# Kernel optimization log

Measured on AMD Instinct MI355X. Metric: run time of the kernel, lower is better.

The kernel has to match this reference:

```python
import jax, jax.numpy as jnp
import numpy as np


def setup_inputs() -> dict:
    key = jax.random.key(0)
    k1, k2, k3, k4 = jax.random.split(key, 4)
    N, E, C_in, C_out = 100000, 1600000, 256, 128
    x = jax.random.normal(k1, (N, C_in), dtype=jnp.float32)
    edge_index = jax.random.randint(k2, (2, E), 0, N, dtype=jnp.int64)
    W = jax.random.normal(k3, (C_in, C_out), dtype=jnp.float32) * 0.05
    b = jax.random.normal(k4, (C_out,), dtype=jnp.float32) * 0.05
    return {"x": x, "edge_index": edge_index, "W": W, "b": b}


def reference(x, edge_index, W, b):
    # GCNConv (PyG defaults): add self-loops, symmetric normalization,
    # linear transform, scatter-sum aggregation, bias; then ReLU (norm=None).
    N = x.shape[0]
    loops = jnp.arange(N, dtype=edge_index.dtype)
    src = jnp.concatenate([edge_index[0], loops])  # [E+N] message sources (x_j)
    dst = jnp.concatenate([edge_index[1], loops])  # [E+N] aggregation targets

    deg = jax.ops.segment_sum(jnp.ones_like(dst, dtype=x.dtype), dst, num_segments=N)
    deg_inv_sqrt = jnp.where(deg > 0, jax.lax.rsqrt(jnp.maximum(deg, 1.0)), 0.0)
    norm = deg_inv_sqrt[src] * deg_inv_sqrt[dst]  # [E+N]

    h = x @ W                                      # [N, C_out]
    msg = h[src] * norm[:, None]                   # [E+N, C_out] gather + scale
    out = jax.ops.segment_sum(msg, dst, num_segments=N) + b  # scatter-add
    return jax.nn.relu(out)
```

## Files before the change

### kernel.cpp

```cpp
#include <hip/hip_runtime.h>


typedef __attribute__((ext_vector_type(8))) short bf16x8;
typedef __attribute__((ext_vector_type(4))) float f32x4;
typedef __attribute__((ext_vector_type(2))) unsigned int u32x2;

__device__ __forceinline__ unsigned short f2bf(float f) {
  unsigned int u = __float_as_uint(f);
  u += 0x7FFFu + ((u >> 16) & 1u);
  return (unsigned short)(u >> 16);
}
__device__ __forceinline__ float bfval(unsigned short h) {
  return __uint_as_float(((unsigned int)h) << 16);
}
__device__ __forceinline__ float bf0(unsigned int u) { return __uint_as_float(u << 16); }
__device__ __forceinline__ float bf1(unsigned int u) { return __uint_as_float(u & 0xFFFF0000u); }

#define EPB 4096
#define MAXB 256

__global__ __launch_bounds__(256) void k_prep_bin(
    const float* __restrict__ W, unsigned short* __restrict__ blob,
    const int* __restrict__ src, const int* __restrict__ dst,
    u32x2* __restrict__ pairs, unsigned int* __restrict__ binTail,
    int E, int nbins, int shift, int cap)
{
  __shared__ u32x2 stg[EPB];
  __shared__ unsigned int lcnt[MAXB], lbase[MAXB], loff[MAXB];

  const int tid = threadIdx.x;
  const int id = blockIdx.x;

  if (id < 128) {
    int g = id * 256 + tid;
    int k = g >> 7, c = g & 127;
    float w = W[g];
    unsigned short hi = f2bf(w);
    unsigned short lo = f2bf(w - bfval(hi));
    int q = k >> 5, kk = k & 31;
    unsigned lin = (unsigned)(c * 64 + kk * 2);
    unsigned swz = lin ^ (((unsigned)(c & 7)) << 4);
    blob[(q * 16384 + swz) >> 1] = hi;
    blob[(q * 16384 + 8192 + swz) >> 1] = lo;
    return;
  }

  const int e0 = (id - 128) * EPB;
  for (int i = tid; i < MAXB; i += 256) { lcnt[i] = 0u; loff[i] = 0u; }
  __syncthreads();

  #pragma unroll
  for (int i = 0; i < EPB / 256; ++i) {
    const int e = e0 + i * 256 + tid;
    u32x2 pr = {0xFFFFFFFFu, 0u};
    if (e < E) {
      int d = __builtin_nontemporal_load(dst + e);
      int s = __builtin_nontemporal_load(src + e);
      pr.x = (unsigned)d; pr.y = (unsigned)s;
      atomicAdd(&lcnt[d >> shift], 1u);
    }
    stg[i * 256 + tid] = pr;
  }
  __syncthreads();

  if (tid < nbins) {
    unsigned c = lcnt[tid];
    lbase[tid] = c ? atomicAdd(&binTail[tid], c) : 0u;
  }
  __syncthreads();

  #pragma unroll
  for (int i = 0; i < EPB / 256; ++i) {
    const u32x2 pr = stg[i * 256 + tid];
    if (pr.x != 0xFFFFFFFFu) {
      const int bin = (int)(pr.x >> shift);
      const unsigned p = lbase[bin] + atomicAdd(&loff[bin], 1u);
      if (p < (unsigned)cap) {
        u32x2 o;
        o.x = pr.x - ((unsigned)bin << shift);
        o.y = pr.y;
        __builtin_nontemporal_store(o, pairs + (size_t)bin * cap + p);
      }
    }
  }
}

__global__ __launch_bounds__(256) void k_gemm_scatter(
    const float* __restrict__ x, const unsigned char* __restrict__ wblob,
    unsigned short* __restrict__ h, int N,
    const u32x2* __restrict__ pairs, const unsigned int* __restrict__ binTail,
    unsigned int* __restrict__ cnt, int* __restrict__ srcs,
    int nbins, int shift, int cap, int gemmB)
{
  __shared__ __align__(16) unsigned char smem[20480];

  const int id = blockIdx.x;
  const int tid = threadIdx.x;

  if (id < nbins) {
    unsigned int* lcnt = (unsigned int*)smem;
    const int bin = id;
    const int bsz = 1 << shift;
    const int nbase = bin << shift;
    const int nn = min(bsz, N - nbase);
    if (nn <= 0) return;
    for (int i = tid; i < bsz; i += 256) lcnt[i] = 0u;
    __syncthreads();
    const int n = min((int)binTail[bin], cap);
    const u32x2* bp = pairs + (size_t)bin * cap;
    for (int p = tid; p < n; p += 256) {
      const u32x2 pr = bp[p];
      const unsigned pos = atomicAdd(&lcnt[pr.x], 1u);
      if (pos < 64)
        srcs[(((size_t)(nbase + pr.x)) << 6) + pos] = (int)pr.y;
    }
    __syncthreads();
    for (int i = tid; i < nn; i += 256) cnt[nbase + i] = lcnt[i];
    return;
  }

  const int idx = id - nbins;
  if (idx >= gemmB) return;

  const int row0 = idx * 32;
  const int lane = tid & 63;
  const int wv = tid >> 6;
  const int mb = wv & 1;
  const int nb = wv >> 1;

  f32x4 acc[4] = {};

  const int ar = tid >> 3;
  const int akk0 = (tid & 7) * 4;
  int arow = row0 + ar; if (arow >= N) arow = N - 1;
  const unsigned aaddr = ((unsigned)(ar * 64 + akk0 * 2)) ^ (((unsigned)(ar & 7)) << 4);

  const int rr = 16 * mb + (lane & 15);
  const unsigned aoff = ((unsigned)(rr * 64 + (lane >> 4) * 16)) ^ (((unsigned)(rr & 7)) << 4);

  for (int q = 0; q < 8; ++q) {
    {
      const f32x4 v = __builtin_nontemporal_load(
          (const f32x4*)(x + (size_t)arow * 256 + q * 32 + akk0));
      unsigned short h0 = f2bf(v[0]), h1 = f2bf(v[1]), h2 = f2bf(v[2]), h3 = f2bf(v[3]);
      unsigned short l0 = f2bf(v[0] - bfval(h0));
      unsigned short l1 = f2bf(v[1] - bfval(h1));
      unsigned short l2 = f2bf(v[2] - bfval(h2));
      unsigned short l3 = f2bf(v[3] - bfval(h3));
      *(uint2*)(smem + 16384 + aaddr) =
          make_uint2((unsigned)h0 | ((unsigned)h1 << 16), (unsigned)h2 | ((unsigned)h3 << 16));
      *(uint2*)(smem + 18432 + aaddr) =
          make_uint2((unsigned)l0 | ((unsigned)l1 << 16), (unsigned)l2 | ((unsigned)l3 << 16));
    }
    {
      const uint4* gb = (const uint4*)(wblob + (size_t)q * 16384);
      uint4* sb = (uint4*)smem;
      uint4 t0 = gb[tid], t1 = gb[tid + 256], t2 = gb[tid + 512], t3 = gb[tid + 768];
      sb[tid] = t0; sb[tid + 256] = t1; sb[tid + 512] = t2; sb[tid + 768] = t3;
    }
    __syncthreads();
    {
      const bf16x8 ah = *(const bf16x8*)(smem + 16384 + aoff);
      const bf16x8 al = *(const bf16x8*)(smem + 18432 + aoff);
      #pragma unroll
      for (int nf = 0; nf < 4; ++nf) {
        const int c = 64 * nb + 16 * nf + (lane & 15);
        const unsigned boff =
            ((unsigned)(c * 64 + (lane >> 4) * 16)) ^ (((unsigned)(c & 7)) << 4);
        const bf16x8 bh = *(const bf16x8*)(smem + boff);
        const bf16x8 bl = *(const bf16x8*)(smem + 8192 + boff);
        acc[nf] = __builtin_amdgcn_mfma_f32_16x16x32_bf16(ah, bh, acc[nf], 0, 0, 0);
        acc[nf] = __builtin_amdgcn_mfma_f32_16x16x32_bf16(ah, bl, acc[nf], 0, 0, 0);
        acc[nf] = __builtin_amdgcn_mfma_f32_16x16x32_bf16(al, bh, acc[nf], 0, 0, 0);
      }
    }
    __syncthreads();
  }

  #pragma unroll
  for (int nf = 0; nf < 4; ++nf) {
    const int col = 64 * nb + 16 * nf + (lane & 15);
    #pragma unroll
    for (int r = 0; r < 4; ++r) {
      const int row = row0 + 16 * mb + 4 * (lane >> 4) + r;
      if (row < N) h[(size_t)row * 128 + col] = f2bf(acc[nf][r]);
    }
  }
}

__global__ __launch_bounds__(256) void k_aggr(
    const unsigned short* __restrict__ h, const int* __restrict__ srcs,
    const unsigned int* __restrict__ cnt,
    const float* __restrict__ b, float* __restrict__ out, int N)
{
  const int wid = (int)(((size_t)blockIdx.x * 256 + threadIdx.x) >> 6);
  if (wid >= N) return;
  const int lane = threadIdx.x & 63;
  const int eg = lane >> 4;
  const int cl = lane & 15;
  const int deg = min((int)cnt[wid], 64);
  const int m = deg + 1;
  const size_t coff = (size_t)(cl << 3);
  const size_t lbase = (size_t)wid << 6;

  float a0 = 0.f, a1 = 0.f, a2 = 0.f, a3 = 0.f, a4 = 0.f, a5 = 0.f, a6 = 0.f, a7 = 0.f;

  for (int base = 0; base < m; base += 64) {
    const int kk = min(64, m - base);
    const int slot = base + lane;
    int sidx = wid;
    if (slot < deg) sidx = srcs[lbase + slot];
    const float sd = rsqrtf((float)(cnt[sidx] + 1u));
    int j = 0;
    for (; j + 8 <= kk; j += 8) {
      const int s0 = __shfl(sidx, j + eg, 64);
      const int s1 = __shfl(sidx, j + 4 + eg, 64);
      const float d0 = __shfl(sd, j + eg, 64);
      const float d1 = __shfl(sd, j + 4 + eg, 64);
      const uint4 v0 = *(const uint4*)(h + ((size_t)s0 << 7) + coff);
      const uint4 v1 = *(const uint4*)(h + ((size_t)s1 << 7) + coff);
      a0 = fmaf(bf0(v0.x), d0, a0); a1 = fmaf(bf1(v0.x), d0, a1);
      a2 = fmaf(bf0(v0.y), d0, a2); a3 = fmaf(bf1(v0.y), d0, a3);
      a4 = fmaf(bf0(v0.z), d0, a4); a5 = fmaf(bf1(v0.z), d0, a5);
      a6 = fmaf(bf0(v0.w), d0, a6); a7 = fmaf(bf1(v0.w), d0, a7);
      a0 = fmaf(bf0(v1.x), d1, a0); a1 = fmaf(bf1(v1.x), d1, a1);
      a2 = fmaf(bf0(v1.y), d1, a2); a3 = fmaf(bf1(v1.y), d1, a3);
      a4 = fmaf(bf0(v1.z), d1, a4); a5 = fmaf(bf1(v1.z), d1, a5);
      a6 = fmaf(bf0(v1.w), d1, a6); a7 = fmaf(bf1(v1.w), d1, a7);
    }
    for (; j < kk; j += 4) {
      const int s0 = __shfl(sidx, j + eg, 64);
      const float d0 = __shfl(sd, j + eg, 64);
      if (j + eg < kk) {
        const uint4 v0 = *(const uint4*)(h + ((size_t)s0 << 7) + coff);
        a0 = fmaf(bf0(v0.x), d0, a0); a1 = fmaf(bf1(v0.x), d0, a1);
        a2 = fmaf(bf0(v0.y), d0, a2); a3 = fmaf(bf1(v0.y), d0, a3);
        a4 = fmaf(bf0(v0.z), d0, a4); a5 = fmaf(bf1(v0.z), d0, a5);
        a6 = fmaf(bf0(v0.w), d0, a6); a7 = fmaf(bf1(v0.w), d0, a7);
      }
    }
  }

  a0 += __shfl_xor(a0, 16, 64); a0 += __shfl_xor(a0, 32, 64);
  a1 += __shfl_xor(a1, 16, 64); a1 += __shfl_xor(a1, 32, 64);
  a2 += __shfl_xor(a2, 16, 64); a2 += __shfl_xor(a2, 32, 64);
  a3 += __shfl_xor(a3, 16, 64); a3 += __shfl_xor(a3, 32, 64);
  a4 += __shfl_xor(a4, 16, 64); a4 += __shfl_xor(a4, 32, 64);
  a5 += __shfl_xor(a5, 16, 64); a5 += __shfl_xor(a5, 32, 64);
  a6 += __shfl_xor(a6, 16, 64); a6 += __shfl_xor(a6, 32, 64);
  a7 += __shfl_xor(a7, 16, 64); a7 += __shfl_xor(a7, 32, 64);

  if (lane < 32) {
    const float dn = rsqrtf((float)m);
    const int hi = lane >> 4;
    const int c0 = ((lane & 15) << 3) + (hi << 2);
    const float4 bb = *(const float4*)(b + c0);
    const float r0 = hi ? a4 : a0;
    const float r1 = hi ? a5 : a1;
    const float r2 = hi ? a6 : a2;
    const float r3 = hi ? a7 : a3;
    float4 o;
    o.x = fmaxf(fmaf(dn, r0, bb.x), 0.f);
    o.y = fmaxf(fmaf(dn, r1, bb.y), 0.f);
    o.z = fmaxf(fmaf(dn, r2, bb.z), 0.f);
    o.w = fmaxf(fmaf(dn, r3, bb.w), 0.f);
    *(float4*)(out + ((size_t)wid << 7) + c0) = o;
  }
}

extern "C" void kernel_launch(void* const* d_in, const int* in_sizes, int n_in,
                              void* d_out, int out_size, void* d_ws, size_t ws_size,
                              hipStream_t stream)
{
  const float* x  = (const float*)d_in[0];
  const int* ei   = (const int*)d_in[1];
  const float* W  = (const float*)d_in[2];
  const float* b  = (const float*)d_in[3];
  float* out = (float*)d_out;

  const int Cout = in_sizes[3];
  const int Cin  = in_sizes[2] / Cout;
  const int N    = in_sizes[0] / Cin;
  const int E    = in_sizes[1] / 2;

  const int* src = ei;
  const int* dst = ei + E;

  int shift = 9;
  while (((N + (1 << shift) - 1) >> shift) > MAXB) ++shift;
  const int nbins = (N + (1 << shift) - 1) >> shift;
  const int cap = E / nbins + E / (2 * nbins) + 1024;

  char* p = (char*)d_ws;
  size_t off = 0;
  auto alloc = [&](size_t bytes) { char* q = p + off; off = (off + bytes + 255) & ~(size_t)255; return q; };
  unsigned int* cnt = (unsigned int*)alloc((size_t)N * 4);
  int* srcs         = (int*)alloc((size_t)N * 64 * 4);
  unsigned short* h = (unsigned short*)alloc((size_t)N * Cout * 2);
  unsigned short* wblob = (unsigned short*)alloc(8 * 16384);
  unsigned int* binTail = (unsigned int*)alloc((size_t)nbins * 4);
  u32x2* pairs      = (u32x2*)alloc((size_t)nbins * cap * 8);

  const int gemmB = (N + 31) / 32;
  const int binB  = (E + EPB - 1) / EPB;

  (void)hipMemsetAsync(binTail, 0, (size_t)nbins * 4, stream);
  k_prep_bin<<<128 + binB, 256, 0, stream>>>(W, wblob, src, dst,
                                             pairs, binTail, E, nbins, shift, cap);
  k_gemm_scatter<<<nbins + gemmB, 256, 0, stream>>>(x, (const unsigned char*)wblob, h, N,
                                                    pairs, binTail, cnt, srcs,
                                                    nbins, shift, cap, gemmB);
  k_aggr<<<(N + 3) / 4, 256, 0, stream>>>(h, srcs, cnt, b, out, N);
}
```

Measured before the change: 337.2 us.

## Fuse memset, prep/bin and gemm/scatter into one cooperative persistent kernel

Merges the binTail memset, the weight-prep/edge-binning kernel and the gemm/bucket kernel into a single cooperative kernel of 1024 persistent blocks, separated by grid-wide syncs. It also splits the per-block bin histogram into per-wavefront copies to reduce LDS atomic contention, and re-reads dst/src from global memory instead of staging edge pairs in LDS. The goal is to remove launch gaps and the memset. In exchange it adds grid barriers and a fixed grid size that may underfill or serialize work, and it keeps the old kernels as a fallback if the cooperative launch fails.

Measured after the change: 691.1 us. 2.05x slower.

```diff
diff --git a/kernel.cpp b/kernel.cpp
--- a/kernel.cpp
+++ b/kernel.cpp
@@ -1,4 +1,7 @@
 #include <hip/hip_runtime.h>
+#include <hip/hip_cooperative_groups.h>
+
+namespace cg = cooperative_groups;
 
 
 typedef __attribute__((ext_vector_type(8))) short bf16x8;
@@ -19,109 +22,50 @@
 #define EPB 4096
 #define MAXB 256
 
-__global__ __launch_bounds__(256) void k_prep_bin(
-    const float* __restrict__ W, unsigned short* __restrict__ blob,
-    const int* __restrict__ src, const int* __restrict__ dst,
-    u32x2* __restrict__ pairs, unsigned int* __restrict__ binTail,
-    int E, int nbins, int shift, int cap)
-{
-  __shared__ u32x2 stg[EPB];
-  __shared__ unsigned int lcnt[MAXB], lbase[MAXB], loff[MAXB];
-
-  const int tid = threadIdx.x;
-  const int id = blockIdx.x;
-
-  if (id < 128) {
-    int g = id * 256 + tid;
-    int k = g >> 7, c = g & 127;
-    float w = W[g];
-    unsigned short hi = f2bf(w);
-    unsigned short lo = f2bf(w - bfval(hi));
-    int q = k >> 5, kk = k & 31;
-    unsigned lin = (unsigned)(c * 64 + kk * 2);
-    unsigned swz = lin ^ (((unsigned)(c & 7)) << 4);
-    blob[(q * 16384 + swz) >> 1] = hi;
-    blob[(q * 16384 + 8192 + swz) >> 1] = lo;
-    return;
-  }
-
-  const int e0 = (id - 128) * EPB;
-  for (int i = tid; i < MAXB; i += 256) { lcnt[i] = 0u; loff[i] = 0u; }
-  __syncthreads();
-
-  #pragma unroll
-  for (int i = 0; i < EPB / 256; ++i) {
-    const int e = e0 + i * 256 + tid;
-    u32x2 pr = {0xFFFFFFFFu, 0u};
-    if (e < E) {
-      int d = __builtin_nontemporal_load(dst + e);
-      int s = __builtin_nontemporal_load(src + e);
-      pr.x = (unsigned)d; pr.y = (unsigned)s;
-      atomicAdd(&lcnt[d >> shift], 1u);
-    }
-    stg[i * 256 + tid] = pr;
-  }
-  __syncthreads();
-
-  if (tid < nbins) {
-    unsigned c = lcnt[tid];
-    lbase[tid] = c ? atomicAdd(&binTail[tid], c) : 0u;
-  }
-  __syncthreads();
-
-  #pragma unroll
-  for (int i = 0; i < EPB / 256; ++i) {
-    const u32x2 pr = stg[i * 256 + tid];
-    if (pr.x != 0xFFFFFFFFu) {
-      const int bin = (int)(pr.x >> shift);
-      const unsigned p = lbase[bin] + atomicAdd(&loff[bin], 1u);
-      if (p < (unsigned)cap) {
-        u32x2 o;
-        o.x = pr.x - ((unsigned)bin << shift);
-        o.y = pr.y;
-        __builtin_nontemporal_store(o, pairs + (size_t)bin * cap + p);
-      }
-    }
-  }
-}
-
-__global__ __launch_bounds__(256) void k_gemm_scatter(
-    const float* __restrict__ x, const unsigned char* __restrict__ wblob,
-    unsigned short* __restrict__ h, int N,
+
+__device__ __forceinline__ void wprep_elem(const float* __restrict__ W,
+                                           unsigned short* __restrict__ blob, int g) {
+  int k = g >> 7, c = g & 127;
+  float w = W[g];
+  unsigned short hi = f2bf(w);
+  unsigned short lo = f2bf(w - bfval(hi));
+  int q = k >> 5, kk = k & 31;
+  unsigned lin = (unsigned)(c * 64 + kk * 2);
+  unsigned swz = lin ^ (((unsigned)(c & 7)) << 4);
+  blob[(q * 16384 + swz) >> 1] = hi;
+  blob[(q * 16384 + 8192 + swz) >> 1] = lo;
+}
+
+__device__ __forceinline__ void bucket_body(
+    unsigned char* smem, int bin, int tid,
     const u32x2* __restrict__ pairs, const unsigned int* __restrict__ binTail,
     unsigned int* __restrict__ cnt, int* __restrict__ srcs,
-    int nbins, int shift, int cap, int gemmB)
-{
-  __shared__ __align__(16) unsigned char smem[20480];
-
-  const int id = blockIdx.x;
-  const int tid = threadIdx.x;
-
-  if (id < nbins) {
-    unsigned int* lcnt = (unsigned int*)smem;
-    const int bin = id;
-    const int bsz = 1 << shift;
-    const int nbase = bin << shift;
-    const int nn = min(bsz, N - nbase);
-    if (nn <= 0) return;
-    for (int i = tid; i < bsz; i += 256) lcnt[i] = 0u;
-    __syncthreads();
-    const int n = min((int)binTail[bin], cap);
-    const u32x2* bp = pairs + (size_t)bin * cap;
-    for (int p = tid; p < n; p += 256) {
-      const u32x2 pr = bp[p];
-      const unsigned pos = atomicAdd(&lcnt[pr.x], 1u);
-      if (pos < 64)
-        srcs[(((size_t)(nbase + pr.x)) << 6) + pos] = (int)pr.y;
-    }
-    __syncthreads();
-    for (int i = tid; i < nn; i += 256) cnt[nbase + i] = lcnt[i];
-    return;
-  }
-
-  const int idx = id - nbins;
-  if (idx >= gemmB) return;
-
+    int N, int shift, int cap)
+{
+  unsigned int* lcnt = (unsigned int*)smem;
+  const int bsz = 1 << shift;
+  const int nbase = bin << shift;
+  const int nn = min(bsz, N - nbase);
+  if (nn <= 0) return;
+  for (int i = tid; i < bsz; i += 256) lcnt[i] = 0u;
+  __syncthreads();
+  const int n = min((int)binTail[bin], cap);
+  const u32x2* bp = pairs + (size_t)bin * cap;
+  for (int p = tid; p < n; p += 256) {
+    const u32x2 pr = bp[p];
+    const unsigned pos = atomicAdd(&lcnt[pr.x], 1u);
+    if (pos < 64)
+      srcs[(((size_t)(nbase + pr.x)) << 6) + pos] = (int)pr.y;
+  }
+  __syncthreads();
+  for (int i = tid; i < nn; i += 256) cnt[nbase + i] = lcnt[i];
+}
+
+__device__ __forceinline__ void gemm_body(
+    unsigned char* smem, int idx, int tid,
+    const float* __restrict__ x, const unsigned char* __restrict__ wblob,
+    unsigned short* __restrict__ h, int N)
+{
   const int row0 = idx * 32;
   const int lane = tid & 63;
   const int wv = tid >> 6;
@@ -186,6 +130,151 @@
       if (row < N) h[(size_t)row * 128 + col] = f2bf(acc[nf][r]);
     }
   }
+}
+
+__global__ __launch_bounds__(256) void k_mega(
+    const float* __restrict__ x, const float* __restrict__ W,
+    const int* __restrict__ src, const int* __restrict__ dst,
+    unsigned short* __restrict__ wblob, u32x2* __restrict__ pairs,
+    unsigned int* __restrict__ binTail, unsigned int* __restrict__ cnt,
+    int* __restrict__ srcs, unsigned short* __restrict__ h,
+    int N, int E, int nbins, int shift, int cap, int prepB, int gemmB)
+{
+  __shared__ __align__(16) unsigned char smem[20480];
+  cg::grid_group grid = cg::this_grid();
+  const int tid = threadIdx.x;
+  const int nblk = (int)gridDim.x;
+  const int gtid = (int)blockIdx.x * 256 + tid;
+  const int gthreads = nblk * 256;
+
+  for (int i = gtid; i < nbins; i += gthreads) binTail[i] = 0u;
+  for (int g = gtid; g < 256 * 128; g += gthreads) wprep_elem(W, wblob, g);
+  __threadfence();
+  grid.sync();
+
+  for (int vb = (int)blockIdx.x; vb < prepB; vb += nblk) {
+    unsigned int* lcnt4 = (unsigned int*)smem;
+    unsigned int* lbase = lcnt4 + 4 * MAXB;
+    unsigned int* loff  = lbase + MAXB;
+    __syncthreads();
+    for (int i = tid; i < 4 * MAXB; i += 256) lcnt4[i] = 0u;
+    for (int i = tid; i < MAXB; i += 256) loff[i] = 0u;
+    __syncthreads();
+    const int e0 = vb * EPB;
+    const int wv = tid >> 6;
+    #pragma unroll
+    for (int i = 0; i < EPB / 256; ++i) {
+      const int e = e0 + i * 256 + tid;
+      if (e < E) {
+        int d = __builtin_nontemporal_load(dst + e);
+        atomicAdd(&lcnt4[wv * MAXB + (d >> shift)], 1u);
+      }
+    }
+    __syncthreads();
+    if (tid < nbins) {
+      unsigned c = lcnt4[tid] + lcnt4[MAXB + tid] + lcnt4[2 * MAXB + tid] + lcnt4[3 * MAXB + tid];
+      lbase[tid] = c ? atomicAdd(&binTail[tid], c) : 0u;
+    }
+    __syncthreads();
+    #pragma unroll
+    for (int i = 0; i < EPB / 256; ++i) {
+      const int e = e0 + i * 256 + tid;
+      if (e < E) {
+        int d = dst[e];
+        int s = src[e];
+        const int bin = d >> shift;
+        const unsigned p = lbase[bin] + atomicAdd(&loff[bin], 1u);
+        if (p < (unsigned)cap) {
+          u32x2 o;
+          o.x = (unsigned)d - ((unsigned)bin << shift);
+          o.y = (unsigned)s;
+          __builtin_nontemporal_store(o, pairs + (size_t)bin * cap + p);
+        }
+      }
+    }
+  }
+  __threadfence();
+  grid.sync();
+
+  for (int vb = (int)blockIdx.x; vb < nbins + gemmB; vb += nblk) {
+    __syncthreads();
+    if (vb < nbins)
+      bucket_body(smem, vb, tid, pairs, binTail, cnt, srcs, N, shift, cap);
+    else
+      gemm_body(smem, vb - nbins, tid, x, (const unsigned char*)wblob, h, N);
+  }
+}
+
+
+__global__ __launch_bounds__(256) void k_prep_bin(
+    const float* __restrict__ W, unsigned short* __restrict__ blob,
+    const int* __restrict__ src, const int* __restrict__ dst,
+    u32x2* __restrict__ pairs, unsigned int* __restrict__ binTail,
+    int E, int nbins, int shift, int cap)
+{
+  __shared__ unsigned int lcnt4[4 * MAXB];
+  __shared__ unsigned int lbase[MAXB], loff[MAXB];
+  const int tid = threadIdx.x;
+  const int id = blockIdx.x;
+
+  if (id < 128) {
+    wprep_elem(W, blob, id * 256 + tid);
+    return;
+  }
+  for (int i = tid; i < 4 * MAXB; i += 256) lcnt4[i] = 0u;
+  for (int i = tid; i < MAXB; i += 256) loff[i] = 0u;
+  __syncthreads();
+  const int e0 = (id - 128) * EPB;
+  const int wv = tid >> 6;
+  #pragma unroll
+  for (int i = 0; i < EPB / 256; ++i) {
+    const int e = e0 + i * 256 + tid;
+    if (e < E) {
+      int d = __builtin_nontemporal_load(dst + e);
+      atomicAdd(&lcnt4[wv * MAXB + (d >> shift)], 1u);
+    }
+  }
+  __syncthreads();
+  if (tid < nbins) {
+    unsigned c = lcnt4[tid] + lcnt4[MAXB + tid] + lcnt4[2 * MAXB + tid] + lcnt4[3 * MAXB + tid];
+    lbase[tid] = c ? atomicAdd(&binTail[tid], c) : 0u;
+  }
+  __syncthreads();
+  #pragma unroll
+  for (int i = 0; i < EPB / 256; ++i) {
+    const int e = e0 + i * 256 + tid;
+    if (e < E) {
+      int d = dst[e];
+      int s = src[e];
+      const int bin = d >> shift;
+      const unsigned p = lbase[bin] + atomicAdd(&loff[bin], 1u);
+      if (p < (unsigned)cap) {
+        u32x2 o;
+        o.x = (unsigned)d - ((unsigned)bin << shift);
+        o.y = (unsigned)s;
+        __builtin_nontemporal_store(o, pairs + (size_t)bin * cap + p);
+      }
+    }
+  }
+}
+
+__global__ __launch_bounds__(256) void k_gemm_scatter(
+    const float* __restrict__ x, const unsigned char* __restrict__ wblob,
+    unsigned short* __restrict__ h, int N,
+    const u32x2* __restrict__ pairs, const unsigned int* __restrict__ binTail,
+    unsigned int* __restrict__ cnt, int* __restrict__ srcs,
+    int nbins, int shift, int cap, int gemmB)
+{
+  __shared__ __align__(16) unsigned char smem[20480];
+  const int id = blockIdx.x;
+  const int tid = threadIdx.x;
+  if (id < nbins) {
+    bucket_body(smem, id, tid, pairs, binTail, cnt, srcs, N, shift, cap);
+    return;
+  }
+  const int idx = id - nbins;
+  if (idx >= gemmB) return;
+  gemm_body(smem, idx, tid, x, wblob, h, N);
 }
 
 __global__ __launch_bounds__(256) void k_aggr(
@@ -302,13 +391,34 @@
   u32x2* pairs      = (u32x2*)alloc((size_t)nbins * cap * 8);
 
   const int gemmB = (N + 31) / 32;
-  const int binB  = (E + EPB - 1) / EPB;
-
-  (void)hipMemsetAsync(binTail, 0, (size_t)nbins * 4, stream);
-  k_prep_bin<<<128 + binB, 256, 0, stream>>>(W, wblob, src, dst,
-                                             pairs, binTail, E, nbins, shift, cap);
-  k_gemm_scatter<<<nbins + gemmB, 256, 0, stream>>>(x, (const unsigned char*)wblob, h, N,
-                                                    pairs, binTail, cnt, srcs,
-                                                    nbins, shift, cap, gemmB);
+  const int prepB = (E + EPB - 1) / EPB;
+
+  {
+    int N_ = N, E_ = E, nbins_ = nbins, shift_ = shift, cap_ = cap;
+    int prepB_ = prepB, gemmB_ = gemmB;
+    const float* x_ = x; const float* W_ = W;
+    const int* src_ = src; const int* dst_ = dst;
+    unsigned short* wblob_ = wblob; u32x2* pairs_ = pairs;
+    unsigned int* binTail_ = binTail; unsigned int* cnt_ = cnt;
+    int* srcs_ = srcs; unsigned short* h_ = h;
+    void* args[] = {
+      (void*)&x_, (void*)&W_, (void*)&src_, (void*)&dst_,
+      (void*)&wblob_, (void*)&pairs_, (void*)&binTail_, (void*)&cnt_,
+      (void*)&srcs_, (void*)&h_,
+      (void*)&N_, (void*)&E_, (void*)&nbins_, (void*)&shift_, (void*)&cap_,
+      (void*)&prepB_, (void*)&gemmB_
+    };
+    hipError_t err = hipLaunchCooperativeKernel((const void*)k_mega,
+                                                dim3(1024), dim3(256),
+                                                args, 0, stream);
+    if (err != hipSuccess) {
+      (void)hipMemsetAsync(binTail, 0, (size_t)nbins * 4, stream);
+      k_prep_bin<<<128 + prepB, 256, 0, stream>>>(W, wblob, src, dst,
+                                                  pairs, binTail, E, nbins, shift, cap);
+      k_gemm_scatter<<<nbins + gemmB, 256, 0, stream>>>(x, (const unsigned char*)wblob, h, N,
+                                                        pairs, binTail, cnt, srcs,
+                                                        nbins, shift, cap, gemmB);
+    }
+  }
   k_aggr<<<(N + 3) / 4, 256, 0, stream>>>(h, srcs, cnt, b, out, N);
 }
```

## Overlap edge binning with GEMM and split bucket pass into separate kernel

Applied to the files above, without the earlier changes.

Moves the edge-binning pass out of the W-prep kernel and co-schedules it with the GEMM blocks in one launch, so the memory-bound binning overlaps the MFMA work. The per-bin bucketing becomes its own kernel with 1024-thread blocks. Binning now keeps per-wave shared counters to reduce atomic contention, re-reads dst/src instead of staging them in LDS, and halves the edges per block. The output store becomes nontemporal. In exchange it adds a kernel launch and reads the edge indices twice.

New measurement: 343.9 us. No clear change (+2.0%).

```diff
diff --git a/kernel.cpp b/kernel.cpp
--- a/kernel.cpp
+++ b/kernel.cpp
@@ -16,110 +16,79 @@
 __device__ __forceinline__ float bf0(unsigned int u) { return __uint_as_float(u << 16); }
 __device__ __forceinline__ float bf1(unsigned int u) { return __uint_as_float(u & 0xFFFF0000u); }
 
-#define EPB 4096
+#define EPB 2048
 #define MAXB 256
 
-__global__ __launch_bounds__(256) void k_prep_bin(
-    const float* __restrict__ W, unsigned short* __restrict__ blob,
+__global__ __launch_bounds__(256) void k_wprep(
+    const float* __restrict__ W, unsigned short* __restrict__ blob)
+{
+  int g = blockIdx.x * 256 + threadIdx.x;
+  int k = g >> 7, c = g & 127;
+  float w = W[g];
+  unsigned short hi = f2bf(w);
+  unsigned short lo = f2bf(w - bfval(hi));
+  int q = k >> 5, kk = k & 31;
+  unsigned lin = (unsigned)(c * 64 + kk * 2);
+  unsigned swz = lin ^ (((unsigned)(c & 7)) << 4);
+  blob[(q * 16384 + swz) >> 1] = hi;
+  blob[(q * 16384 + 8192 + swz) >> 1] = lo;
+}
+
+__global__ __launch_bounds__(256) void k_work(
+    const float* __restrict__ x, const unsigned char* __restrict__ wblob,
+    unsigned short* __restrict__ h, int N,
     const int* __restrict__ src, const int* __restrict__ dst,
     u32x2* __restrict__ pairs, unsigned int* __restrict__ binTail,
-    int E, int nbins, int shift, int cap)
-{
-  __shared__ u32x2 stg[EPB];
-  __shared__ unsigned int lcnt[MAXB], lbase[MAXB], loff[MAXB];
-
-  const int tid = threadIdx.x;
-  const int id = blockIdx.x;
-
-  if (id < 128) {
-    int g = id * 256 + tid;
-    int k = g >> 7, c = g & 127;
-    float w = W[g];
-    unsigned short hi = f2bf(w);
-    unsigned short lo = f2bf(w - bfval(hi));
-    int q = k >> 5, kk = k & 31;
-    unsigned lin = (unsigned)(c * 64 + kk * 2);
-    unsigned swz = lin ^ (((unsigned)(c & 7)) << 4);
-    blob[(q * 16384 + swz) >> 1] = hi;
-    blob[(q * 16384 + 8192 + swz) >> 1] = lo;
-    return;
-  }
-
-  const int e0 = (id - 128) * EPB;
-  for (int i = tid; i < MAXB; i += 256) { lcnt[i] = 0u; loff[i] = 0u; }
-  __syncthreads();
-
-  #pragma unroll
-  for (int i = 0; i < EPB / 256; ++i) {
-    const int e = e0 + i * 256 + tid;
-    u32x2 pr = {0xFFFFFFFFu, 0u};
-    if (e < E) {
-      int d = __builtin_nontemporal_load(dst + e);
-      int s = __builtin_nontemporal_load(src + e);
-      pr.x = (unsigned)d; pr.y = (unsigned)s;
-      atomicAdd(&lcnt[d >> shift], 1u);
-    }
-    stg[i * 256 + tid] = pr;
-  }
-  __syncthreads();
-
-  if (tid < nbins) {
-    unsigned c = lcnt[tid];
-    lbase[tid] = c ? atomicAdd(&binTail[tid], c) : 0u;
-  }
-  __syncthreads();
-
-  #pragma unroll
-  for (int i = 0; i < EPB / 256; ++i) {
-    const u32x2 pr = stg[i * 256 + tid];
-    if (pr.x != 0xFFFFFFFFu) {
-      const int bin = (int)(pr.x >> shift);
-      const unsigned p = lbase[bin] + atomicAdd(&loff[bin], 1u);
-      if (p < (unsigned)cap) {
-        u32x2 o;
-        o.x = pr.x - ((unsigned)bin << shift);
-        o.y = pr.y;
-        __builtin_nontemporal_store(o, pairs + (size_t)bin * cap + p);
-      }
-    }
-  }
-}
-
-__global__ __launch_bounds__(256) void k_gemm_scatter(
-    const float* __restrict__ x, const unsigned char* __restrict__ wblob,
-    unsigned short* __restrict__ h, int N,
-    const u32x2* __restrict__ pairs, const unsigned int* __restrict__ binTail,
-    unsigned int* __restrict__ cnt, int* __restrict__ srcs,
-    int nbins, int shift, int cap, int gemmB)
+    int E, int nbins, int shift, int cap, int binB, int gemmB)
 {
   __shared__ __align__(16) unsigned char smem[20480];
 
   const int id = blockIdx.x;
   const int tid = threadIdx.x;
 
-  if (id < nbins) {
-    unsigned int* lcnt = (unsigned int*)smem;
-    const int bin = id;
-    const int bsz = 1 << shift;
-    const int nbase = bin << shift;
-    const int nn = min(bsz, N - nbase);
-    if (nn <= 0) return;
-    for (int i = tid; i < bsz; i += 256) lcnt[i] = 0u;
-    __syncthreads();
-    const int n = min((int)binTail[bin], cap);
-    const u32x2* bp = pairs + (size_t)bin * cap;
-    for (int p = tid; p < n; p += 256) {
-      const u32x2 pr = bp[p];
-      const unsigned pos = atomicAdd(&lcnt[pr.x], 1u);
-      if (pos < 64)
-        srcs[(((size_t)(nbase + pr.x)) << 6) + pos] = (int)pr.y;
-    }
-    __syncthreads();
-    for (int i = tid; i < nn; i += 256) cnt[nbase + i] = lcnt[i];
+  if (id < binB) {
+    unsigned int* lcnt4 = (unsigned int*)smem;
+    unsigned int* lbase = lcnt4 + 4 * MAXB;
+    unsigned int* loff  = lbase + MAXB;
+    for (int i = tid; i < 4 * MAXB; i += 256) lcnt4[i] = 0u;
+    for (int i = tid; i < MAXB; i += 256) loff[i] = 0u;
+    __syncthreads();
+    const int e0 = id * EPB;
+    const int wv = tid >> 6;
+    #pragma unroll
+    for (int i = 0; i < EPB / 256; ++i) {
+      const int e = e0 + i * 256 + tid;
+      if (e < E) {
+        int d = dst[e];
+        atomicAdd(&lcnt4[wv * MAXB + (d >> shift)], 1u);
+      }
+    }
+    __syncthreads();
+    if (tid < nbins) {
+      unsigned c = lcnt4[tid] + lcnt4[MAXB + tid] + lcnt4[2 * MAXB + tid] + lcnt4[3 * MAXB + tid];
+      lbase[tid] = c ? atomicAdd(&binTail[tid], c) : 0u;
+    }
+    __syncthreads();
+    #pragma unroll
+    for (int i = 0; i < EPB / 256; ++i) {
+      const int e = e0 + i * 256 + tid;
+      if (e < E) {
+        int d = dst[e];
+        int s = src[e];
+        const int bin = d >> shift;
+        const unsigned p = lbase[bin] + atomicAdd(&loff[bin], 1u);
+        if (p < (unsigned)cap) {
+          u32x2 o;
+          o.x = (unsigned)d - ((unsigned)bin << shift);
+          o.y = (unsigned)s;
+          __builtin_nontemporal_store(o, pairs + (size_t)bin * cap + p);
+        }
+      }
+    }
     return;
   }
 
-  const int idx = id - nbins;
+  const int idx = id - binB;
   if (idx >= gemmB) return;
 
   const int row0 = idx * 32;
@@ -186,6 +155,32 @@
       if (row < N) h[(size_t)row * 128 + col] = f2bf(acc[nf][r]);
     }
   }
+}
+
+__global__ __launch_bounds__(1024) void k_bucket(
+    const u32x2* __restrict__ pairs, const unsigned int* __restrict__ binTail,
+    unsigned int* __restrict__ cnt, int* __restrict__ srcs,
+    int N, int shift, int cap)
+{
+  __shared__ unsigned int lcnt[1 << 9];
+  const int bin = blockIdx.x;
+  const int tid = threadIdx.x;
+  const int bsz = 1 << shift;
+  const int nbase = bin << shift;
+  const int nn = min(bsz, N - nbase);
+  if (nn <= 0) return;
+  for (int i = tid; i < bsz; i += 1024) lcnt[i] = 0u;
+  __syncthreads();
+  const int n = min((int)binTail[bin], cap);
+  const u32x2* bp = pairs + (size_t)bin * cap;
+  for (int p = tid; p < n; p += 1024) {
+    const u32x2 pr = __builtin_nontemporal_load(bp + p);
+    const unsigned pos = atomicAdd(&lcnt[pr.x], 1u);
+    if (pos < 64)
+      srcs[(((size_t)(nbase + pr.x)) << 6) + pos] = (int)pr.y;
+  }
+  __syncthreads();
+  for (int i = tid; i < nn; i += 1024) cnt[nbase + i] = lcnt[i];
 }
 
 __global__ __launch_bounds__(256) void k_aggr(
@@ -259,12 +254,12 @@
     const float r1 = hi ? a5 : a1;
     const float r2 = hi ? a6 : a2;
     const float r3 = hi ? a7 : a3;
-    float4 o;
-    o.x = fmaxf(fmaf(dn, r0, bb.x), 0.f);
-    o.y = fmaxf(fmaf(dn, r1, bb.y), 0.f);
-    o.z = fmaxf(fmaf(dn, r2, bb.z), 0.f);
-    o.w = fmaxf(fmaf(dn, r3, bb.w), 0.f);
-    *(float4*)(out + ((size_t)wid << 7) + c0) = o;
+    f32x4 o;
+    o[0] = fmaxf(fmaf(dn, r0, bb.x), 0.f);
+    o[1] = fmaxf(fmaf(dn, r1, bb.y), 0.f);
+    o[2] = fmaxf(fmaf(dn, r2, bb.z), 0.f);
+    o[3] = fmaxf(fmaf(dn, r3, bb.w), 0.f);
+    __builtin_nontemporal_store(o, (f32x4*)(out + ((size_t)wid << 7) + c0));
   }
 }
 
@@ -305,10 +300,10 @@
   const int binB  = (E + EPB - 1) / EPB;
 
   (void)hipMemsetAsync(binTail, 0, (size_t)nbins * 4, stream);
-  k_prep_bin<<<128 + binB, 256, 0, stream>>>(W, wblob, src, dst,
-                                             pairs, binTail, E, nbins, shift, cap);
-  k_gemm_scatter<<<nbins + gemmB, 256, 0, stream>>>(x, (const unsigned char*)wblob, h, N,
-                                                    pairs, binTail, cnt, srcs,
-                                                    nbins, shift, cap, gemmB);
+  k_wprep<<<128, 256, 0, stream>>>(W, wblob);
+  k_work<<<binB + gemmB, 256, 0, stream>>>(x, (const unsigned char*)wblob, h, N,
+                                           src, dst, pairs, binTail,
+                                           E, nbins, shift, cap, binB, gemmB);
+  k_bucket<<<nbins, 1024, 0, stream>>>(pairs, binTail, cnt, srcs, N, shift, cap);
   k_aggr<<<(N + 3) / 4, 256, 0, stream>>>(h, srcs, cnt, b, out, N);
 }
```
